# Kernel tuning notes

Hardware: AMD Instinct MI355X
Metric: run time of the kernel (lower is better)

## Reference

```python
import jax, jax.numpy as jnp
import numpy as np

TEMP = 0.07  # init temperature
EPS = 1e-12  # F.normalize eps


def _per_cloud_loss(fmap, labels):
    # fmap: [C, N] per-point features; labels: [N] int
    v = fmap.T  # [N, C]
    v = v / jnp.maximum(jnp.linalg.norm(v, axis=1, keepdims=True), EPS)
    # NxN similarity, exp then divide by temp (order matches original)
    dot = jnp.exp(v @ v.T) / TEMP  # [N, N]
    dot = dot - jnp.diag(jnp.diag(dot))  # zero the diagonal
    mask = (labels[:, None] == labels[None, :]).astype(dot.dtype)  # [N, N]
    mask_not = 1.0 - mask
    pos = (mask * dot).sum(1) / mask.sum(1)  # note: denom includes self, as in original
    neg = (mask_not * dot).sum(1) / mask_not.sum(1)
    return jnp.mean(-jnp.log(pos / (pos + neg)))


def setup_inputs() -> dict:
    key = jax.random.key(0)
    k1, k2 = jax.random.split(key)
    B, C, N = 8, 128, 4096
    features = jax.random.normal(k1, (B, C, N), dtype=jnp.float32)
    labels_all = jax.random.randint(k2, (B, N), 0, 16, dtype=jnp.int64)
    return {"features": features, "labels_all": labels_all}


def reference(features, labels_all):
    losses = jax.vmap(_per_cloud_loss)(features, labels_all)  # [B]
    return jnp.mean(losses)
```

## Files before the change

### kernel.cpp

```cpp
#include <hip/hip_runtime.h>
#include <stdint.h>

#define NPTS 4096
#define NC 128
#define NB 8
#define CSPLIT 8
#define COLS_PER (NPTS / CSPLIT)
#define RPB 128

typedef __bf16 bf16x8 __attribute__((ext_vector_type(8)));
typedef float f32x4 __attribute__((ext_vector_type(4)));
typedef unsigned short u16;
typedef unsigned int u32;
typedef unsigned long long u64;

__device__ inline float fast_exp2(float x) { return __builtin_amdgcn_exp2f(x); }

__device__ inline u16 f2bf(float x) {
    u32 u = __float_as_uint(x);
    u32 r = (u + 0x7fffu + ((u >> 16) & 1u)) >> 16;
    return (u16)r;
}

typedef __attribute__((address_space(1))) const void glb_void;
typedef __attribute__((address_space(3))) void lds_void;
__device__ inline void gload_lds16(const void* g, void* l) {
    __builtin_amdgcn_global_load_lds((glb_void*)g, (lds_void*)l, 16, 0, 0);
}

__global__ __launch_bounds__(256) void hist_kernel(const int* __restrict__ labels,
                                                   int* __restrict__ counts,
                                                   int* __restrict__ baseg,
                                                   u32* __restrict__ zb) {
    int b = blockIdx.x, tid = threadIdx.x;
    if (b == 0 && tid < 2) zb[tid] = 0u;
    __shared__ int cnt[64][16];
    __shared__ int tot[16];
    for (int i = tid; i < 64 * 16; i += 256) ((int*)cnt)[i] = 0;
    __syncthreads();
    for (int n = tid; n < NPTS; n += 256)
        atomicAdd(&cnt[n >> 6][labels[b * NPTS + n] & 15], 1);
    __syncthreads();
    if (tid < 16) {
        int s = 0;
        for (int k = 0; k < 64; ++k) s += cnt[k][tid];
        counts[b * 16 + tid] = s;
        tot[tid] = s;
    }
    __syncthreads();
    if (tid == 0) {
        int run = 0;
        for (int l = 0; l < 16; ++l) { int c = tot[l]; tot[l] = run; run += c; }
    }
    __syncthreads();
    if (tid < 16) {
        int run = tot[tid];
        for (int k = 0; k < 64; ++k) {
            baseg[(b * 64 + k) * 16 + tid] = run;
            run += cnt[k][tid];
        }
    }
}

__global__ __launch_bounds__(256) void norm_kernel(const float* __restrict__ feat,
                                                   const int* __restrict__ labels,
                                                   const int* __restrict__ baseg,
                                                   u16* __restrict__ vbf,
                                                   int* __restrict__ slab) {
    int b = blockIdx.y;
    int blk = blockIdx.x;
    int tid = threadIdx.x;
    int n0 = blk * 64;
    __shared__ float tile[64][129];
    __shared__ float part[8][64];
    __shared__ float rn[64];
    __shared__ int lpos[64];
    const float* fb = feat + (size_t)b * NC * NPTS;
    int nslot = tid & 31;
    int ty = tid >> 5;
    float s0 = 0.f, s1 = 0.f;
#pragma unroll
    for (int i = 0; i < 16; ++i) {
        int c = i * 8 + ty;
        float2 x = *(const float2*)(fb + (size_t)c * NPTS + n0 + 2 * nslot);
        tile[2 * nslot][c] = x.x;
        tile[2 * nslot + 1][c] = x.y;
        s0 += x.x * x.x;
        s1 += x.y * x.y;
    }
    part[ty][2 * nslot] = s0;
    part[ty][2 * nslot + 1] = s1;
    __syncthreads();
    if (tid < 64) {
        float s = 0.f;
#pragma unroll
        for (int t = 0; t < 8; ++t) s += part[t][tid];
        rn[tid] = 1.f / fmaxf(sqrtf(s), 1e-12f);
        int myl = labels[b * NPTS + n0 + tid] & 15;
        u64 mymask = 0ull;
#pragma unroll
        for (int L = 0; L < 16; ++L) {
            u64 bl = __ballot(myl == L);
            if (myl == L) mymask = bl;
        }
        int rank = __popcll(mymask & ((1ull << tid) - 1ull));
        int pos = baseg[(b * 64 + blk) * 16 + myl] + rank;
        lpos[tid] = pos;
        slab[b * NPTS + pos] = myl;
    }
    __syncthreads();
    u32* out = (u32*)vbf;
#pragma unroll
    for (int i = 0; i < 16; ++i) {
        int idx = tid + i * 256;
        int p = idx >> 6, k = idx & 63;
        float r = rn[p];
        float x0 = tile[p][2 * k] * r;
        float x1 = tile[p][2 * k + 1] * r;
        out[((size_t)b * NPTS + lpos[p]) * 64 + k] = (u32)f2bf(x0) | ((u32)f2bf(x1) << 16);
    }
}

__global__ __launch_bounds__(256, 2) void sim_kernel(const u16* __restrict__ vbf,
                                                     const int* __restrict__ slab,
                                                     float2* __restrict__ rowacc) {
    int bid = blockIdx.x;
    int rt = bid >> 6;
    int combo = bid & 63;
    int b = combo >> 3;
    int cs = combo & 7;
    int row0 = rt * RPB;
    int c0 = cs * COLS_PER;
    int tid = threadIdx.x;
    int wave = tid >> 6, lane = tid & 63;
    int quad = lane >> 4, ln = lane & 15;

    const u16* vb = vbf + (size_t)b * NPTS * NC;
    const int* lab = slab + b * NPTS;

    int rbase[2];
    rbase[0] = row0 + wave * 32;
    rbase[1] = rbase[0] + 16;

    bf16x8 afrag[2][4];
#pragma unroll
    for (int s = 0; s < 2; ++s)
#pragma unroll
        for (int f = 0; f < 4; ++f) {
            bf16x8 v = *(const bf16x8*)(vb + (size_t)(rbase[s] + ln) * NC + f * 32 + quad * 8);
#pragma unroll
            for (int k = 0; k < 8; ++k) v[k] = (__bf16)((float)v[k] * 1.44269504f);
            afrag[s][f] = v;
        }

    int lrow[2][4];
#pragma unroll
    for (int s = 0; s < 2; ++s)
#pragma unroll
        for (int r = 0; r < 4; ++r) lrow[s][r] = lab[rbase[s] + quad * 4 + r];

    int row_uni[2];
#pragma unroll
    for (int s = 0; s < 2; ++s) row_uni[s] = (lab[rbase[s]] == lab[rbase[s] + 15]);

    int diagct[2], diagsub[2];
#pragma unroll
    for (int s = 0; s < 2; ++s) {
        diagct[s] = rbase[s] & ~63;
        diagsub[s] = (rbase[s] >> 4) & 3;
    }

    float psame[2][4] = {{0.f}}, pneg[2][4] = {{0.f}};

    __shared__ u16 cols[2][64 * 128];
    __shared__ int clabs[512];
    clabs[tid] = lab[c0 + tid];
    clabs[tid + 256] = lab[c0 + 256 + tid];

    const uint4* src = (const uint4*)(vb + (size_t)c0 * NC);
    int g4[4];
#pragma unroll
    for (int i = 0; i < 4; ++i) {
        int idx16 = (wave * 4 + i) * 64 + lane;
        int rr = idx16 >> 4;
        int cc = (idx16 & 15) ^ (rr & 15);
        g4[i] = rr * 16 + cc;
    }

    int cur = 0;
#pragma unroll
    for (int i = 0; i < 4; ++i)
        gload_lds16(src + g4[i], cols[0] + (wave * 4 + i) * 512);

    for (int t = 0; t < COLS_PER / 64; ++t) {
        __syncthreads();
        if (t < COLS_PER / 64 - 1) {
#pragma unroll
            for (int i = 0; i < 4; ++i)
                gload_lds16(src + (t + 1) * 1024 + g4[i], cols[cur ^ 1] + (wave * 4 + i) * 512);
        }
        int ct = c0 + t * 64;

#pragma unroll
        for (int sub = 0; sub < 4; ++sub) {
            const u16* rowb = cols[cur] + (sub * 16 + ln) * 128;
            bf16x8 bfrag[4];
#pragma unroll
            for (int f = 0; f < 4; ++f)
                bfrag[f] = *(const bf16x8*)(rowb + (((4 * f + quad) ^ ln) * 8));
            int lc = clabs[t * 64 + sub * 16 + ln];
            int clo = __shfl(lc, 0), chi = __shfl(lc, 15);
#pragma unroll
            for (int s = 0; s < 2; ++s) {
                f32x4 d = {0.f, 0.f, 0.f, 0.f};
#pragma unroll
                for (int f = 0; f < 4; ++f)
                    d = __builtin_amdgcn_mfma_f32_16x16x32_bf16(afrag[s][f], bfrag[f], d, 0, 0, 0);
                if (ct == diagct[s] && sub == diagsub[s]) {
#pragma unroll
                    for (int r = 0; r < 4; ++r) {
                        float e = fast_exp2(d[r]);
                        if (ln == quad * 4 + r) e = 0.f;
                        bool m = (lc == lrow[s][r]);
                        psame[s][r] += m ? e : 0.f;
                        pneg[s][r] += m ? 0.f : e;
                    }
                } else if (row_uni[s] && clo == chi) {
                    if (clo == lrow[s][0]) {
#pragma unroll
                        for (int r = 0; r < 4; ++r) psame[s][r] += fast_exp2(d[r]);
                    } else {
#pragma unroll
                        for (int r = 0; r < 4; ++r) pneg[s][r] += fast_exp2(d[r]);
                    }
                } else {
#pragma unroll
                    for (int r = 0; r < 4; ++r) {
                        float e = fast_exp2(d[r]);
                        bool m = (lc == lrow[s][r]);
                        psame[s][r] += m ? e : 0.f;
                        pneg[s][r] += m ? 0.f : e;
                    }
                }
            }
        }
        cur ^= 1;
    }

#pragma unroll
    for (int off = 1; off < 16; off <<= 1)
#pragma unroll
        for (int s = 0; s < 2; ++s)
#pragma unroll
            for (int r = 0; r < 4; ++r) {
                psame[s][r] += __shfl_xor(psame[s][r], off);
                pneg[s][r] += __shfl_xor(pneg[s][r], off);
            }
    if (ln == 0) {
#pragma unroll
        for (int s = 0; s < 2; ++s)
#pragma unroll
            for (int r = 0; r < 4; ++r)
                rowacc[((size_t)cs * NB + b) * NPTS + rbase[s] + quad * 4 + r] =
                    make_float2(psame[s][r], pneg[s][r]);
    }
}

__global__ __launch_bounds__(256) void loss_kernel(const float2* __restrict__ rowacc,
                                                   const int* __restrict__ slab,
                                                   const int* __restrict__ counts,
                                                   float* __restrict__ acc,
                                                   u32* __restrict__ ticket,
                                                   float* __restrict__ out) {
    int idx = blockIdx.x * 256 + threadIdx.x;
    int b = idx >> 12;
    float ps = 0.f, pn = 0.f;
#pragma unroll
    for (int cs = 0; cs < CSPLIT; ++cs) {
        float2 v = rowacc[(size_t)cs * NB * NPTS + idx];
        ps += v.x;
        pn += v.y;
    }
    int lb = slab[idx] & 15;
    int cnt = counts[b * 16 + lb];
    float p = ps / (float)cnt;
    float n = pn / (float)(NPTS - cnt);
    float loss = -__logf(p / (p + n));
#pragma unroll
    for (int off = 1; off < 64; off <<= 1) loss += __shfl_xor(loss, off);
    __shared__ float w[4];
    if ((threadIdx.x & 63) == 0) w[threadIdx.x >> 6] = loss;
    __syncthreads();
    if (threadIdx.x == 0) {
        atomicAdd(acc, w[0] + w[1] + w[2] + w[3]);
        __threadfence();
        u32 t = atomicAdd(ticket, 1u);
        if (t == gridDim.x - 1) {
            float v = atomicAdd(acc, 0.f);
            out[0] = v * (1.f / (float)(NB * NPTS));
        }
    }
}

extern "C" void kernel_launch(void* const* d_in, const int* in_sizes, int n_in,
                              void* d_out, int out_size, void* d_ws, size_t ws_size,
                              hipStream_t stream) {
    const float* feat = (const float*)d_in[0];
    const int* labels = (const int*)d_in[1];
    float* out = (float*)d_out;

    float* acc = (float*)d_ws;
    u32* ticket = (u32*)((char*)d_ws + 4);
    int* counts = (int*)((char*)d_ws + 256);
    int* baseg = (int*)((char*)d_ws + 1024);
    int* slab = (int*)((char*)d_ws + 36864);
    float2* rowacc = (float2*)((char*)d_ws + 172032);
    u16* vbf = (u16*)((char*)d_ws + 172032 + (size_t)CSPLIT * NB * NPTS * 8);

    hist_kernel<<<dim3(NB), 256, 0, stream>>>(labels, counts, baseg, (u32*)d_ws);
    norm_kernel<<<dim3(64, NB), 256, 0, stream>>>(feat, labels, baseg, vbf, slab);
    sim_kernel<<<dim3(32 * 64), 256, 0, stream>>>(vbf, slab, rowacc);
    loss_kernel<<<dim3(NB * NPTS / 256), 256, 0, stream>>>(rowacc, slab, counts, acc, ticket, out);
}
```

Before: 131.5 us.

## Double rows per block, split columns 16-way, atomically accumulate row sums

Each sim block now handles 256 rows (four 16-row subtiles per wave) against 256 columns. Each loaded column tile is reused across more A fragments, and the grid keeps the same block count. Per-split partial row sums are combined with float atomics into a single buffer cleared by a memset, so the loss kernel reads one value per row. Row labels are packed into bytes and the uniform-label fast path is broadened using label range checks on sorted labels. The change raises register pressure (launch bounds drop to 1 block per SM), adds atomic traffic and an extra memset launch, and makes the float summation order nondeterministic.

```diff
diff --git a/kernel.cpp b/kernel.cpp
--- a/kernel.cpp
+++ b/kernel.cpp
@@ -4,9 +4,10 @@
 #define NPTS 4096
 #define NC 128
 #define NB 8
-#define CSPLIT 8
+#define CSPLIT 16
 #define COLS_PER (NPTS / CSPLIT)
-#define RPB 128
+#define TILES (COLS_PER / 64)
+#define RPB 256
 
 typedef __bf16 bf16x8 __attribute__((ext_vector_type(8)));
 typedef float f32x4 __attribute__((ext_vector_type(4)));
@@ -121,14 +122,14 @@
     }
 }
 
-__global__ __launch_bounds__(256, 2) void sim_kernel(const u16* __restrict__ vbf,
+__global__ __launch_bounds__(256, 1) void sim_kernel(const u16* __restrict__ vbf,
                                                      const int* __restrict__ slab,
-                                                     float2* __restrict__ rowacc) {
+                                                     float* __restrict__ rowaccf) {
     int bid = blockIdx.x;
-    int rt = bid >> 6;
-    int combo = bid & 63;
-    int b = combo >> 3;
-    int cs = combo & 7;
+    int rt = bid >> 7;
+    int combo = bid & 127;
+    int b = combo >> 4;
+    int cs = combo & 15;
     int row0 = rt * RPB;
     int c0 = cs * COLS_PER;
     int tid = threadIdx.x;
@@ -138,13 +139,13 @@
     const u16* vb = vbf + (size_t)b * NPTS * NC;
     const int* lab = slab + b * NPTS;
 
-    int rbase[2];
-    rbase[0] = row0 + wave * 32;
-    rbase[1] = rbase[0] + 16;
-
-    bf16x8 afrag[2][4];
-#pragma unroll
-    for (int s = 0; s < 2; ++s)
+    int rbase[4];
+#pragma unroll
+    for (int s = 0; s < 4; ++s) rbase[s] = row0 + wave * 64 + s * 16;
+
+    bf16x8 afrag[4][4];
+#pragma unroll
+    for (int s = 0; s < 4; ++s)
 #pragma unroll
         for (int f = 0; f < 4; ++f) {
             bf16x8 v = *(const bf16x8*)(vb + (size_t)(rbase[s] + ln) * NC + f * 32 + quad * 8);
@@ -153,29 +154,31 @@
             afrag[s][f] = v;
         }
 
-    int lrow[2][4];
-#pragma unroll
-    for (int s = 0; s < 2; ++s)
-#pragma unroll
-        for (int r = 0; r < 4; ++r) lrow[s][r] = lab[rbase[s] + quad * 4 + r];
-
-    int row_uni[2];
-#pragma unroll
-    for (int s = 0; s < 2; ++s) row_uni[s] = (lab[rbase[s]] == lab[rbase[s] + 15]);
-
-    int diagct[2], diagsub[2];
-#pragma unroll
-    for (int s = 0; s < 2; ++s) {
+    int lrp[4];
+#pragma unroll
+    for (int s = 0; s < 4; ++s) {
+        int base = rbase[s] + quad * 4;
+        lrp[s] = lab[base] | (lab[base + 1] << 8) | (lab[base + 2] << 16) | (lab[base + 3] << 24);
+    }
+    int slo[4], shi[4];
+#pragma unroll
+    for (int s = 0; s < 4; ++s) {
+        slo[s] = __builtin_amdgcn_readfirstlane(lab[rbase[s]]);
+        shi[s] = __builtin_amdgcn_readfirstlane(lab[rbase[s] + 15]);
+    }
+
+    int diagct[4], diagsub[4];
+#pragma unroll
+    for (int s = 0; s < 4; ++s) {
         diagct[s] = rbase[s] & ~63;
         diagsub[s] = (rbase[s] >> 4) & 3;
     }
 
-    float psame[2][4] = {{0.f}}, pneg[2][4] = {{0.f}};
+    float psame[4][4] = {{0.f}}, pneg[4][4] = {{0.f}};
 
     __shared__ u16 cols[2][64 * 128];
-    __shared__ int clabs[512];
+    __shared__ int clabs[COLS_PER];
     clabs[tid] = lab[c0 + tid];
-    clabs[tid + 256] = lab[c0 + 256 + tid];
 
     const uint4* src = (const uint4*)(vb + (size_t)c0 * NC);
     int g4[4];
@@ -192,9 +195,9 @@
     for (int i = 0; i < 4; ++i)
         gload_lds16(src + g4[i], cols[0] + (wave * 4 + i) * 512);
 
-    for (int t = 0; t < COLS_PER / 64; ++t) {
+    for (int t = 0; t < TILES; ++t) {
         __syncthreads();
-        if (t < COLS_PER / 64 - 1) {
+        if (t < TILES - 1) {
 #pragma unroll
             for (int i = 0; i < 4; ++i)
                 gload_lds16(src + (t + 1) * 1024 + g4[i], cols[cur ^ 1] + (wave * 4 + i) * 512);
@@ -208,36 +211,47 @@
 #pragma unroll
             for (int f = 0; f < 4; ++f)
                 bfrag[f] = *(const bf16x8*)(rowb + (((4 * f + quad) ^ ln) * 8));
-            int lc = clabs[t * 64 + sub * 16 + ln];
-            int clo = __shfl(lc, 0), chi = __shfl(lc, 15);
-#pragma unroll
-            for (int s = 0; s < 2; ++s) {
+            int cbase = t * 64 + sub * 16;
+            int clo = __builtin_amdgcn_readfirstlane(clabs[cbase]);
+            int chi = __builtin_amdgcn_readfirstlane(clabs[cbase + 15]);
+#pragma unroll
+            for (int s = 0; s < 4; ++s) {
                 f32x4 d = {0.f, 0.f, 0.f, 0.f};
 #pragma unroll
                 for (int f = 0; f < 4; ++f)
                     d = __builtin_amdgcn_mfma_f32_16x16x32_bf16(afrag[s][f], bfrag[f], d, 0, 0, 0);
                 if (ct == diagct[s] && sub == diagsub[s]) {
+                    int lc = clabs[cbase + ln];
 #pragma unroll
                     for (int r = 0; r < 4; ++r) {
                         float e = fast_exp2(d[r]);
                         if (ln == quad * 4 + r) e = 0.f;
-                        bool m = (lc == lrow[s][r]);
+                        bool m = (((lrp[s] >> (8 * r)) & 255) == lc);
                         psame[s][r] += m ? e : 0.f;
                         pneg[s][r] += m ? 0.f : e;
                     }
-                } else if (row_uni[s] && clo == chi) {
-                    if (clo == lrow[s][0]) {
+                } else if (clo == chi) {
+                    if (clo < slo[s] || clo > shi[s]) {
+#pragma unroll
+                        for (int r = 0; r < 4; ++r) pneg[s][r] += fast_exp2(d[r]);
+                    } else if (slo[s] == shi[s]) {
 #pragma unroll
                         for (int r = 0; r < 4; ++r) psame[s][r] += fast_exp2(d[r]);
                     } else {
 #pragma unroll
-                        for (int r = 0; r < 4; ++r) pneg[s][r] += fast_exp2(d[r]);
+                        for (int r = 0; r < 4; ++r) {
+                            float e = fast_exp2(d[r]);
+                            bool m = (((lrp[s] >> (8 * r)) & 255) == clo);
+                            psame[s][r] += m ? e : 0.f;
+                            pneg[s][r] += m ? 0.f : e;
+                        }
                     }
                 } else {
+                    int lc = clabs[cbase + ln];
 #pragma unroll
                     for (int r = 0; r < 4; ++r) {
                         float e = fast_exp2(d[r]);
-                        bool m = (lc == lrow[s][r]);
+                        bool m = (((lrp[s] >> (8 * r)) & 255) == lc);
                         psame[s][r] += m ? e : 0.f;
                         pneg[s][r] += m ? 0.f : e;
                     }
@@ -250,7 +264,7 @@
 #pragma unroll
     for (int off = 1; off < 16; off <<= 1)
 #pragma unroll
-        for (int s = 0; s < 2; ++s)
+        for (int s = 0; s < 4; ++s)
 #pragma unroll
             for (int r = 0; r < 4; ++r) {
                 psame[s][r] += __shfl_xor(psame[s][r], off);
@@ -258,11 +272,13 @@
             }
     if (ln == 0) {
 #pragma unroll
-        for (int s = 0; s < 2; ++s)
-#pragma unroll
-            for (int r = 0; r < 4; ++r)
-                rowacc[((size_t)cs * NB + b) * NPTS + rbase[s] + quad * 4 + r] =
-                    make_float2(psame[s][r], pneg[s][r]);
+        for (int s = 0; s < 4; ++s)
+#pragma unroll
+            for (int r = 0; r < 4; ++r) {
+                size_t o = 2 * ((size_t)b * NPTS + rbase[s] + quad * 4 + r);
+                atomicAdd(rowaccf + o, psame[s][r]);
+                atomicAdd(rowaccf + o + 1, pneg[s][r]);
+            }
     }
 }
 
@@ -274,13 +290,8 @@
                                                    float* __restrict__ out) {
     int idx = blockIdx.x * 256 + threadIdx.x;
     int b = idx >> 12;
-    float ps = 0.f, pn = 0.f;
-#pragma unroll
-    for (int cs = 0; cs < CSPLIT; ++cs) {
-        float2 v = rowacc[(size_t)cs * NB * NPTS + idx];
-        ps += v.x;
-        pn += v.y;
-    }
+    float2 v = rowacc[idx];
+    float ps = v.x, pn = v.y;
     int lb = slab[idx] & 15;
     int cnt = counts[b * 16 + lb];
     float p = ps / (float)cnt;
@@ -296,8 +307,8 @@
         __threadfence();
         u32 t = atomicAdd(ticket, 1u);
         if (t == gridDim.x - 1) {
-            float v = atomicAdd(acc, 0.f);
-            out[0] = v * (1.f / (float)(NB * NPTS));
+            float v2 = atomicAdd(acc, 0.f);
+            out[0] = v2 * (1.f / (float)(NB * NPTS));
         }
     }
 }
@@ -314,11 +325,13 @@
     int* counts = (int*)((char*)d_ws + 256);
     int* baseg = (int*)((char*)d_ws + 1024);
     int* slab = (int*)((char*)d_ws + 36864);
-    float2* rowacc = (float2*)((char*)d_ws + 172032);
-    u16* vbf = (u16*)((char*)d_ws + 172032 + (size_t)CSPLIT * NB * NPTS * 8);
-
+    float* rowaccf = (float*)((char*)d_ws + 172032);
+    u16* vbf = (u16*)((char*)d_ws + 172032 + (size_t)NB * NPTS * 8);
+
+    hipMemsetAsync(rowaccf, 0, (size_t)NB * NPTS * 2 * sizeof(float), stream);
     hist_kernel<<<dim3(NB), 256, 0, stream>>>(labels, counts, baseg, (u32*)d_ws);
     norm_kernel<<<dim3(64, NB), 256, 0, stream>>>(feat, labels, baseg, vbf, slab);
-    sim_kernel<<<dim3(32 * 64), 256, 0, stream>>>(vbf, slab, rowacc);
-    loss_kernel<<<dim3(NB * NPTS / 256), 256, 0, stream>>>(rowacc, slab, counts, acc, ticket, out);
-}
+    sim_kernel<<<dim3(16 * 128), 256, 0, stream>>>(vbf, slab, rowaccf);
+    loss_kernel<<<dim3(NB * NPTS / 256), 256, 0, stream>>>((const float2*)rowaccf, slab, counts,
+                                                           acc, ticket, out);
+}
```

New measurement: 239.3 us. 1.82x slower.
